# Optimization experiments

Measured on AMD Instinct MI355X. Metric: run time of the kernel, lower is better.

The kernel has to match this reference:

```python
import jax, jax.numpy as jnp
import numpy as np

MODES = 2
LC = 4
N = 6000
KNN = 10
NODES = 64
CH = MODES ** 2
M = N * 2 * (KNN + 1)  # total candidate couplings


def setup_inputs() -> dict:
    key = jax.random.key(0)
    ks = jax.random.split(key, 6)
    return {
        "CK_inputs": jax.random.normal(ks[0], (N, 2 * (KNN + 1), 3), dtype=jnp.float32),
        "W_in": jax.random.normal(ks[1], (3, NODES), dtype=jnp.float32) * 0.1,
        "b_in": jnp.zeros((NODES,), dtype=jnp.float32),
        "W_hid": jax.random.normal(ks[2], (LC - 1, NODES, NODES), dtype=jnp.float32) * 0.1,
        "b_hid": jnp.zeros((LC - 1, NODES), dtype=jnp.float32),
        "W_out": jax.random.normal(ks[3], (NODES, CH), dtype=jnp.float32) * 0.1,
        "b_out": jnp.zeros((CH,), dtype=jnp.float32),
        "coo": jax.random.randint(ks[4], (2, M), 0, N, dtype=jnp.int32),
    }


def _mlp(x, W_in, b_in, W_hid, b_hid, W_out, b_out):
    # MLP: 3 -> 64, (LC-1) hidden 64->64 layers, 64 -> CH; ReLU activations.
    h = jax.nn.relu(x @ W_in + b_in)
    for i in range(W_hid.shape[0]):  # small fixed layer count
        h = jax.nn.relu(h @ W_hid[i] + b_hid[i])
    return h @ W_out + b_out  # [M, CH]


def reference(CK_inputs, W_in, b_in, W_hid, b_hid, W_out, b_out, coo):
    C_stripped = _mlp(CK_inputs.reshape(-1, 3), W_in, b_in, W_hid, b_hid, W_out, b_out)  # [M, CH]
    D = MODES * N
    # Original: for channel ch = mi*MODES+mj, scatter C_stripped[:, ch] at indices coo*MODES+mj
    # (mj added to BOTH row and col, replicating the source exactly). Indices are
    # independent of mi, so sum over mi first, then one scatter-add per mj.
    vals = C_stripped.reshape(-1, MODES, MODES).sum(axis=1)  # [M, MODES]; axis1=mi, axis2=mj
    dense = jnp.zeros((D, D), dtype=CK_inputs.dtype)
    for mj in range(MODES):
        idx = coo * MODES + mj  # [2, M]
        dense = dense.at[idx[0], idx[1]].add(vals[:, mj])
    return dense
```

## Files before the change

kernel.cpp:

```cpp
#include <hip/hip_runtime.h>
#include <stdint.h>

#define NN    6000
#define KNNC  10
#define MM    (NN * 2 * (KNNC + 1))
#define DD    (2 * NN)
#define LCH   3
#define BLK   256

#define RB     128
#define RPL    2
#define MLPB   1032
#define FILLB  2064
#define GRID   (MLPB + FILLB)
#define NV     ((long long)DD * DD / 4)
#define SCGRID ((MM + BLK - 1) / BLK)

__global__ __launch_bounds__(BLK, 4) void fused_fill_mlp(
    const float* __restrict__ CK,
    const float* __restrict__ Win,
    const float* __restrict__ bin,
    const float* __restrict__ Whid,
    const float* __restrict__ bhid,
    const float* __restrict__ Wout,
    const float* __restrict__ bout,
    float* __restrict__ vals,
    float* __restrict__ out)
{
    __shared__ float sH[64 * RB];

    const int bid = blockIdx.x;
    const int tid = threadIdx.x;

    if (bid % 3 != 2) {
        const int fid = (bid / 3) * 2 + (bid % 3);
        long long i = (long long)fid * BLK + tid;
        const long long stride = (long long)FILLB * BLK;
        float4 z = make_float4(0.f, 0.f, 0.f, 0.f);
        float4* outv = (float4*)out;
        for (; i < NV; i += stride) outv[i] = z;
        return;
    }

    const int wave = tid >> 6;
    const int lane = tid & 63;
    const int jo = __builtin_amdgcn_readfirstlane((tid >> 6) << 4);

    const int rbase = (bid / 3) * RB;
    const int mb0   = rbase + lane * 2;
    const int mb    = mb0 < MM ? mb0 : MM - 2;

    const float2 ca = *(const float2*)(CK + mb * 3);
    const float2 cb = *(const float2*)(CK + mb * 3 + 2);
    const float2 cc = *(const float2*)(CK + mb * 3 + 4);
    const float x0[RPL] = {ca.x, cb.y};
    const float x1[RPL] = {ca.y, cc.x};
    const float x2[RPL] = {cb.x, cc.y};

#pragma unroll
    for (int jj = 0; jj < 16; jj++) {
        const int j = jo + jj;
        const float w0 = Win[j], w1 = Win[64 + j], w2 = Win[128 + j];
        const float bj = bin[j];
        float2 hv;
        hv.x = fmaxf(fmaf(x2[0], w2, fmaf(x1[0], w1, fmaf(x0[0], w0, bj))), 0.f);
        hv.y = fmaxf(fmaf(x2[1], w2, fmaf(x1[1], w1, fmaf(x0[1], w0, bj))), 0.f);
        *(float2*)(sH + j * RB + lane * 2) = hv;
    }
    __syncthreads();

#pragma unroll 1
    for (int l = 0; l < LCH; l++) {
        const float* __restrict__ Wl = Whid + (l << 12) + jo;
        const float* __restrict__ bh = bhid + (l << 6) + jo;

        float g[RPL][16];
#pragma unroll
        for (int jj = 0; jj < 16; jj++) {
            const float bj = bh[jj];
            g[0][jj] = bj;
            g[1][jj] = bj;
        }

#pragma unroll 4
        for (int k = 0; k < 64; k++) {
            const float4 wa = *(const float4*)(Wl + (k << 6));
            const float4 wb = *(const float4*)(Wl + (k << 6) + 4);
            const float4 wc = *(const float4*)(Wl + (k << 6) + 8);
            const float4 wd = *(const float4*)(Wl + (k << 6) + 12);
            const float2 hv = *(const float2*)(sH + k * RB + lane * 2);
            const float hk[RPL] = {hv.x, hv.y};
#pragma unroll
            for (int r = 0; r < RPL; r++) {
                g[r][0]  = fmaf(wa.x, hk[r], g[r][0]);
                g[r][1]  = fmaf(wa.y, hk[r], g[r][1]);
                g[r][2]  = fmaf(wa.z, hk[r], g[r][2]);
                g[r][3]  = fmaf(wa.w, hk[r], g[r][3]);
                g[r][4]  = fmaf(wb.x, hk[r], g[r][4]);
                g[r][5]  = fmaf(wb.y, hk[r], g[r][5]);
                g[r][6]  = fmaf(wb.z, hk[r], g[r][6]);
                g[r][7]  = fmaf(wb.w, hk[r], g[r][7]);
                g[r][8]  = fmaf(wc.x, hk[r], g[r][8]);
                g[r][9]  = fmaf(wc.y, hk[r], g[r][9]);
                g[r][10] = fmaf(wc.z, hk[r], g[r][10]);
                g[r][11] = fmaf(wc.w, hk[r], g[r][11]);
                g[r][12] = fmaf(wd.x, hk[r], g[r][12]);
                g[r][13] = fmaf(wd.y, hk[r], g[r][13]);
                g[r][14] = fmaf(wd.z, hk[r], g[r][14]);
                g[r][15] = fmaf(wd.w, hk[r], g[r][15]);
            }
        }
        __syncthreads();

#pragma unroll
        for (int jj = 0; jj < 16; jj++) {
            float2 hv;
            hv.x = fmaxf(g[0][jj], 0.f);
            hv.y = fmaxf(g[1][jj], 0.f);
            *(float2*)(sH + (jo + jj) * RB + lane * 2) = hv;
        }
        __syncthreads();
    }

    float v0[RPL], v1[RPL];
    const float b02 = bout[0] + bout[2], b13 = bout[1] + bout[3];
#pragma unroll
    for (int r = 0; r < RPL; r++) { v0[r] = b02; v1[r] = b13; }
#pragma unroll 8
    for (int k = 0; k < 64; k++) {
        const float4 wo = ((const float4*)Wout)[k];
        const float wxz = wo.x + wo.z, wyw = wo.y + wo.w;
        const float2 hv = *(const float2*)(sH + k * RB + lane * 2);
        v0[0] = fmaf(hv.x, wxz, v0[0]);  v1[0] = fmaf(hv.x, wyw, v1[0]);
        v0[1] = fmaf(hv.y, wxz, v0[1]);  v1[1] = fmaf(hv.y, wyw, v1[1]);
    }
    if (wave == 0 && mb0 < MM) {
        *(float4*)(vals + 2 * mb0) = make_float4(v0[0], v1[0], v0[1], v1[1]);
    }
}

__global__ __launch_bounds__(BLK) void scatter_add(
    const float* __restrict__ vals,
    const int* __restrict__ coo,
    float* __restrict__ out)
{
    const int t = blockIdx.x * BLK + threadIdx.x;
    if (t >= MM) return;
    const int r2 = coo[t] * 2;
    const int c2 = coo[MM + t] * 2;
    const float2 v = *(const float2*)(vals + 2 * t);
    const long long f0 = (long long)r2 * DD + c2;
    unsafeAtomicAdd(out + f0, v.x);
    unsafeAtomicAdd(out + f0 + DD + 1, v.y);
}

extern "C" void kernel_launch(void* const* d_in, const int* in_sizes, int n_in,
                              void* d_out, int out_size, void* d_ws, size_t ws_size,
                              hipStream_t stream) {
    const float* CK   = (const float*)d_in[0];
    const float* Win  = (const float*)d_in[1];
    const float* bin  = (const float*)d_in[2];
    const float* Whid = (const float*)d_in[3];
    const float* bhid = (const float*)d_in[4];
    const float* Wout = (const float*)d_in[5];
    const float* bout = (const float*)d_in[6];
    const int* coo    = (const int*)d_in[7];
    float* out        = (float*)d_out;
    float* vals       = (float*)d_ws;

    fused_fill_mlp<<<GRID, BLK, 0, stream>>>(
        CK, Win, bin, Whid, bhid, Wout, bout, vals, out);
    scatter_add<<<SCGRID, BLK, 0, stream>>>(vals, coo, out);
}
```

Measured before the change: 650.2 us.

## Bin couplings by row and build dense output rows in shared memory

Replaces the full-matrix zero fill and the global atomic scatter-add with a counting-bin pass. While the MLP stores its values, it appends each coupling index to a per-row bin. A per-row kernel then accumulates two output rows in LDS and writes each row to global memory once. This removes the separate zeroing pass and the scattered global atomics. In exchange the MLP no longer overlaps with the fill, bins are capped at a fixed size per row, and the new path depends on having enough workspace.

```diff
diff --git a/kernel.cpp b/kernel.cpp
--- a/kernel.cpp
+++ b/kernel.cpp
@@ -10,13 +10,23 @@
 
 #define RB     128
 #define RPL    2
-#define MLPB   1032
-#define FILLB  2064
-#define GRID   (MLPB + FILLB)
-#define NV     ((long long)DD * DD / 4)
-#define SCGRID ((MM + BLK - 1) / BLK)
-
-__global__ __launch_bounds__(BLK, 4) void fused_fill_mlp(
+#define MLPGRID ((MM + RB - 1) / RB)
+#define SCGRID  ((MM + BLK - 1) / BLK)
+#define OUTBYTES ((size_t)DD * DD * 4)
+
+#define MAXB     128
+#define VALS_B   (MM * 2 * 4)
+#define CNT_B    (NN * 4)
+#define BINS_B   (NN * MAXB * 4)
+#define WS_NEEDED (VALS_B + CNT_B + BINS_B)
+
+
+__global__ void zero_cnt(int* __restrict__ cnt) {
+    const int i = blockIdx.x * BLK + threadIdx.x;
+    if (i < NN) cnt[i] = 0;
+}
+
+__global__ __launch_bounds__(BLK, 4) void mlp_bin(
     const float* __restrict__ CK,
     const float* __restrict__ Win,
     const float* __restrict__ bin,
@@ -24,29 +34,20 @@
     const float* __restrict__ bhid,
     const float* __restrict__ Wout,
     const float* __restrict__ bout,
+    const int* __restrict__ coo,
     float* __restrict__ vals,
-    float* __restrict__ out)
+    int* __restrict__ cnt,
+    int* __restrict__ bins,
+    const int do_bins)
 {
     __shared__ float sH[64 * RB];
 
-    const int bid = blockIdx.x;
-    const int tid = threadIdx.x;
-
-    if (bid % 3 != 2) {
-        const int fid = (bid / 3) * 2 + (bid % 3);
-        long long i = (long long)fid * BLK + tid;
-        const long long stride = (long long)FILLB * BLK;
-        float4 z = make_float4(0.f, 0.f, 0.f, 0.f);
-        float4* outv = (float4*)out;
-        for (; i < NV; i += stride) outv[i] = z;
-        return;
-    }
-
+    const int tid  = threadIdx.x;
     const int wave = tid >> 6;
     const int lane = tid & 63;
     const int jo = __builtin_amdgcn_readfirstlane((tid >> 6) << 4);
 
-    const int rbase = (bid / 3) * RB;
+    const int rbase = blockIdx.x * RB;
     const int mb0   = rbase + lane * 2;
     const int mb    = mb0 < MM ? mb0 : MM - 2;
 
@@ -136,12 +137,52 @@
     }
     if (wave == 0 && mb0 < MM) {
         *(float4*)(vals + 2 * mb0) = make_float4(v0[0], v1[0], v0[1], v1[1]);
-    }
-}
-
-__global__ __launch_bounds__(BLK) void scatter_add(
+        if (do_bins) {
+#pragma unroll
+            for (int r = 0; r < RPL; r++) {
+                const int m = mb0 + r;
+                const int i = coo[m];
+                const int pos = atomicAdd(&cnt[i], 1);
+                if (pos < MAXB) bins[i * MAXB + pos] = m;
+            }
+        }
+    }
+}
+
+__global__ __launch_bounds__(BLK, 3) void fill_place(
     const float* __restrict__ vals,
     const int* __restrict__ coo,
+    const int* __restrict__ cnt,
+    const int* __restrict__ bins,
+    float* __restrict__ out)
+{
+    __shared__ float row[DD];
+
+    const int i   = blockIdx.x;
+    const int tid = threadIdx.x;
+    int n = cnt[i];
+    if (n > MAXB) n = MAXB;
+    if (n < 0)    n = 0;
+
+#pragma unroll 1
+    for (int mj = 0; mj < 2; mj++) {
+        float4 z = make_float4(0.f, 0.f, 0.f, 0.f);
+        for (int j = tid; j < DD / 4; j += BLK) ((float4*)row)[j] = z;
+        __syncthreads();
+        for (int e = tid; e < n; e += BLK) {
+            const int m = bins[i * MAXB + e];
+            const int c = coo[MM + m] * 2 + mj;
+            atomicAdd(&row[c], vals[2 * m + mj]);
+        }
+        __syncthreads();
+        float4* __restrict__ dst = (float4*)(out + (size_t)(2 * i + mj) * DD);
+        for (int j = tid; j < DD / 4; j += BLK) dst[j] = ((const float4*)row)[j];
+        __syncthreads();
+    }
+}
+
+__global__ __launch_bounds__(BLK) void scatter_add(
+    const float* __restrict__ vals, const int* __restrict__ coo,
     float* __restrict__ out)
 {
     const int t = blockIdx.x * BLK + threadIdx.x;
@@ -168,7 +209,17 @@
     float* out        = (float*)d_out;
     float* vals       = (float*)d_ws;
 
-    fused_fill_mlp<<<GRID, BLK, 0, stream>>>(
-        CK, Win, bin, Whid, bhid, Wout, bout, vals, out);
-    scatter_add<<<SCGRID, BLK, 0, stream>>>(vals, coo, out);
-}
+    if (ws_size >= (size_t)WS_NEEDED) {
+        int* cnt  = (int*)((char*)d_ws + VALS_B);
+        int* bins = (int*)((char*)d_ws + VALS_B + CNT_B);
+        zero_cnt<<<(NN + BLK - 1) / BLK, BLK, 0, stream>>>(cnt);
+        mlp_bin<<<MLPGRID, BLK, 0, stream>>>(
+            CK, Win, bin, Whid, bhid, Wout, bout, coo, vals, cnt, bins, 1);
+        fill_place<<<NN, BLK, 0, stream>>>(vals, coo, cnt, bins, out);
+    } else {
+        hipMemsetAsync(out, 0, OUTBYTES, stream);
+        mlp_bin<<<MLPGRID, BLK, 0, stream>>>(
+            CK, Win, bin, Whid, bhid, Wout, bout, coo, vals, nullptr, nullptr, 0);
+        scatter_add<<<SCGRID, BLK, 0, stream>>>(vals, coo, out);
+    }
+}
```

Result: no change. 648.0 us (-0.3%).

## Split zero-fill and scatter into row chunks to keep atomics cache-resident

Applied to the files above, without the earlier changes.

Drops the fused fill+MLP kernel and runs a standalone MLP kernel first. The output is then zeroed in four row-chunks with hipMemsetAsync, and after each memset a scatter kernel adds only the couplings whose row falls in that chunk. The aim is for each chunk's atomic adds to land in lines still held in cache (a chunk is about 144MB) instead of going back to DRAM. In exchange it launches four full scatter grids that each re-read coo, and it loses the overlap between fill and MLP.

```diff
diff --git a/kernel.cpp b/kernel.cpp
--- a/kernel.cpp
+++ b/kernel.cpp
@@ -10,13 +10,15 @@
 
 #define RB     128
 #define RPL    2
-#define MLPB   1032
-#define FILLB  2064
-#define GRID   (MLPB + FILLB)
-#define NV     ((long long)DD * DD / 4)
-#define SCGRID ((MM + BLK - 1) / BLK)
+#define MLPGRID ((MM + RB - 1) / RB)
+#define SCGRID  ((MM + BLK - 1) / BLK)
 
-__global__ __launch_bounds__(BLK, 4) void fused_fill_mlp(
+#define NCHUNK  4
+#define ICHUNK  (NN / NCHUNK)
+#define CHUNKB  ((size_t)ICHUNK * 2 * DD * 4)
+
+
+__global__ __launch_bounds__(BLK, 4) void mlp(
     const float* __restrict__ CK,
     const float* __restrict__ Win,
     const float* __restrict__ bin,
@@ -24,29 +26,16 @@
     const float* __restrict__ bhid,
     const float* __restrict__ Wout,
     const float* __restrict__ bout,
-    float* __restrict__ vals,
-    float* __restrict__ out)
+    float* __restrict__ vals)
 {
     __shared__ float sH[64 * RB];
 
-    const int bid = blockIdx.x;
-    const int tid = threadIdx.x;
-
-    if (bid % 3 != 2) {
-        const int fid = (bid / 3) * 2 + (bid % 3);
-        long long i = (long long)fid * BLK + tid;
-        const long long stride = (long long)FILLB * BLK;
-        float4 z = make_float4(0.f, 0.f, 0.f, 0.f);
-        float4* outv = (float4*)out;
-        for (; i < NV; i += stride) outv[i] = z;
-        return;
-    }
-
+    const int tid  = threadIdx.x;
     const int wave = tid >> 6;
     const int lane = tid & 63;
     const int jo = __builtin_amdgcn_readfirstlane((tid >> 6) << 4);
 
-    const int rbase = (bid / 3) * RB;
+    const int rbase = blockIdx.x * RB;
     const int mb0   = rbase + lane * 2;
     const int mb    = mb0 < MM ? mb0 : MM - 2;
 
@@ -139,17 +128,19 @@
     }
 }
 
-__global__ __launch_bounds__(BLK) void scatter_add(
+__global__ __launch_bounds__(BLK) void patch_chunk(
     const float* __restrict__ vals,
     const int* __restrict__ coo,
-    float* __restrict__ out)
+    float* __restrict__ out,
+    const int i0, const int i1)
 {
     const int t = blockIdx.x * BLK + threadIdx.x;
     if (t >= MM) return;
-    const int r2 = coo[t] * 2;
+    const int i = coo[t];
+    if (i < i0 || i >= i1) return;
     const int c2 = coo[MM + t] * 2;
     const float2 v = *(const float2*)(vals + 2 * t);
-    const long long f0 = (long long)r2 * DD + c2;
+    const long long f0 = (long long)(i * 2) * DD + c2;
     unsafeAtomicAdd(out + f0, v.x);
     unsafeAtomicAdd(out + f0 + DD + 1, v.y);
 }
@@ -168,7 +159,12 @@
     float* out        = (float*)d_out;
     float* vals       = (float*)d_ws;
 
-    fused_fill_mlp<<<GRID, BLK, 0, stream>>>(
-        CK, Win, bin, Whid, bhid, Wout, bout, vals, out);
-    scatter_add<<<SCGRID, BLK, 0, stream>>>(vals, coo, out);
+    mlp<<<MLPGRID, BLK, 0, stream>>>(CK, Win, bin, Whid, bhid, Wout, bout, vals);
+
+    for (int c = 0; c < NCHUNK; c++) {
+        float* slice = out + (size_t)c * ICHUNK * 2 * DD;
+        hipMemsetAsync(slice, 0, CHUNKB, stream);
+        patch_chunk<<<SCGRID, BLK, 0, stream>>>(
+            vals, coo, out, c * ICHUNK, (c + 1) * ICHUNK);
+    }
 }
```

New measurement: 657.5 us. About the same (+1.1%).
